# Kernel tuning notes

Measured on AMD Instinct MI355X. Metric: run time of the kernel, lower is better.

## Reference

```python
import jax, jax.numpy as jnp
import numpy as np

DIM = 512
HEADS = 8
HEAD_DIM = DIM // HEADS
SCALE = HEAD_DIM ** -0.5
B, N = 2, 4096


def setup_inputs() -> dict:
    key = jax.random.key(0)
    ks = jax.random.split(key, 7)
    s = DIM ** -0.5
    return {
        "x": jax.random.normal(ks[0], (B, N, DIM), dtype=jnp.float32),
        "qkv_w": jax.random.normal(ks[1], (DIM, 3 * DIM), dtype=jnp.float32) * s,
        "qkv_b": jax.random.normal(ks[2], (3 * DIM,), dtype=jnp.float32) * 0.01,
        "proj_w": jax.random.normal(ks[3], (DIM, DIM), dtype=jnp.float32) * s,
        "proj_b": jax.random.normal(ks[4], (DIM,), dtype=jnp.float32) * 0.01,
        "gate_w": jax.random.normal(ks[5], (DIM, HEADS), dtype=jnp.float32) * s,
        "gate_b": jax.random.normal(ks[6], (HEADS,), dtype=jnp.float32) * 0.01,
    }


def reference(x, qkv_w, qkv_b, proj_w, proj_b, gate_w, gate_b):
    b, n, c = x.shape
    qkv = x @ qkv_w + qkv_b                       # [B,N,3C]
    qkv = qkv.reshape(b, n, 3, HEADS, HEAD_DIM)
    qkv = jnp.transpose(qkv, (2, 0, 3, 1, 4))     # [3,B,H,N,hd]
    q, k, v = qkv[0], qkv[1], qkv[2]
    attn = jnp.einsum('bhnd,bhmd->bhnm', q, k) * SCALE
    attn = jax.nn.softmax(attn, axis=-1)
    y = jnp.einsum('bhnm,bhmd->bhnd', attn, v)    # [B,H,N,hd]
    gate = jax.nn.sigmoid(x @ gate_w + gate_b)    # [B,N,H] headwise
    gate = jnp.transpose(gate[..., None], (0, 2, 1, 3))  # [B,H,N,1]
    y = y * gate
    y = jnp.transpose(y, (0, 2, 1, 3)).reshape(b, n, c)
    return y @ proj_w + proj_b
```

## Files before the change

kernel.cpp:

```cpp
#include <hip/hip_runtime.h>
#include <hip/hip_bf16.h>

#define BATCH 2
#define NSEQ 4096
#define DIM 512
#define HEADS 8
#define HD 64
#define SCALE 0.125f
#define MROWS (BATCH * NSEQ)

typedef __attribute__((ext_vector_type(8))) short bf16x8;
typedef __attribute__((ext_vector_type(4))) float f32x4;

__device__ __forceinline__ short f2bf(float x) {
    unsigned u = __float_as_uint(x);
    u = (u + 0x7FFFu + ((u >> 16) & 1u)) >> 16;
    return (short)u;
}
__device__ __forceinline__ float bf2f(short s) {
    return __uint_as_float(((unsigned)(unsigned short)s) << 16);
}

__global__ __launch_bounds__(256)
void cast_kernel(const float* __restrict__ in, short* __restrict__ out) {
    const int i = (blockIdx.x * 256 + threadIdx.x) * 4;
    const float4 v = *(const float4*)(in + i);
    short4 o;
    o.x = f2bf(v.x); o.y = f2bf(v.y); o.z = f2bf(v.z); o.w = f2bf(v.w);
    *(short4*)(out + i) = o;
}

__global__ __launch_bounds__(256)
void transpose_cast_kernel(const float* __restrict__ in, short* __restrict__ out,
                           int R, int C) {
    __shared__ float tile[32][33];
    const int n0 = blockIdx.x * 32;
    const int k0 = blockIdx.y * 32;
    const int tx = threadIdx.x, ty = threadIdx.y;
    #pragma unroll
    for (int j = 0; j < 4; ++j)
        tile[ty * 4 + j][tx] = in[(size_t)(k0 + ty * 4 + j) * C + n0 + tx];
    __syncthreads();
    #pragma unroll
    for (int j = 0; j < 4; ++j)
        out[(size_t)(n0 + ty * 4 + j) * R + k0 + tx] = f2bf(tile[tx][ty * 4 + j]);
}

template<int BF16OUT>
__global__ __launch_bounds__(256)
void gemm_mfma_kernel(const short* __restrict__ A, const short* __restrict__ WT,
                      const float* __restrict__ bias,
                      float* __restrict__ C, short* __restrict__ Cb,
                      int N, int K) {
    const int m0 = blockIdx.x * 128;
    const int n0 = blockIdx.y * 128;
    const int t  = threadIdx.x;
    const int w  = t >> 6;
    const int l  = t & 63;
    const int lr = l & 15;
    const int lg = l >> 4;
    const int wm = w >> 1;
    const int wn = w & 1;

    __shared__ short As[128][72];
    __shared__ short Bs[128][72];

    f32x4 acc[4][4];
    #pragma unroll
    for (int fm = 0; fm < 4; ++fm)
        #pragma unroll
        for (int fn = 0; fn < 4; ++fn)
            acc[fm][fn] = (f32x4){0.f, 0.f, 0.f, 0.f};

    for (int k0 = 0; k0 < K; k0 += 64) {
        __syncthreads();
        #pragma unroll
        for (int i = 0; i < 4; ++i) {
            const int s   = t + i * 256;
            const int row = s >> 3, ch = s & 7;
            *(bf16x8*)&As[row][ch * 8] =
                *(const bf16x8*)(A + (size_t)(m0 + row) * K + k0 + ch * 8);
            *(bf16x8*)&Bs[row][ch * 8] =
                *(const bf16x8*)(WT + (size_t)(n0 + row) * K + k0 + ch * 8);
        }
        __syncthreads();

        #pragma unroll
        for (int kc = 0; kc < 2; ++kc) {
            bf16x8 af[4], bf[4];
            #pragma unroll
            for (int f = 0; f < 4; ++f) {
                af[f] = *(const bf16x8*)&As[wm * 64 + f * 16 + lr][kc * 32 + lg * 8];
                bf[f] = *(const bf16x8*)&Bs[wn * 64 + f * 16 + lr][kc * 32 + lg * 8];
            }
            #pragma unroll
            for (int fm = 0; fm < 4; ++fm)
                #pragma unroll
                for (int fn = 0; fn < 4; ++fn)
                    acc[fm][fn] = __builtin_amdgcn_mfma_f32_16x16x32_bf16(
                        af[fm], bf[fn], acc[fm][fn], 0, 0, 0);
        }
    }

    #pragma unroll
    for (int fm = 0; fm < 4; ++fm)
        #pragma unroll
        for (int fn = 0; fn < 4; ++fn) {
            const int col = n0 + wn * 64 + fn * 16 + lr;
            const float bb = bias[col];
            #pragma unroll
            for (int reg = 0; reg < 4; ++reg) {
                const int row = m0 + wm * 64 + fm * 16 + lg * 4 + reg;
                const float v = acc[fm][fn][reg] + bb;
                if (BF16OUT) Cb[(size_t)row * N + col] = f2bf(v);
                else         C [(size_t)row * N + col] = v;
            }
        }
}

__global__ __launch_bounds__(256)
void gate_kernel(const float* __restrict__ x, const float* __restrict__ gw,
                 const float* __restrict__ gb, float* __restrict__ gate) {
    __shared__ float gws[DIM * HEADS];
    const int t = threadIdx.x;
    #pragma unroll
    for (int i = 0; i < DIM * HEADS / (256 * 4); ++i) {
        const int s = (t + i * 256) * 4;
        *(float4*)&gws[s] = *(const float4*)(gw + s);
    }
    __syncthreads();

    const int idx = blockIdx.x * blockDim.x + t;
    const int h   = idx & 7;
    const int row = idx >> 3;
    const float* xr = x + (size_t)row * DIM;
    float acc = 0.f;
    #pragma unroll 4
    for (int k = 0; k < DIM; k += 4) {
        float4 xv = *(const float4*)(xr + k);
        acc = fmaf(xv.x, gws[(k + 0) * HEADS + h], acc);
        acc = fmaf(xv.y, gws[(k + 1) * HEADS + h], acc);
        acc = fmaf(xv.z, gws[(k + 2) * HEADS + h], acc);
        acc = fmaf(xv.w, gws[(k + 3) * HEADS + h], acc);
    }
    acc += gb[h];
    gate[idx] = 1.f / (1.f + __expf(-acc));
}

__global__ __launch_bounds__(256)
void attn_kernel(const short* __restrict__ qkvb, const float* __restrict__ gate,
                 short* __restrict__ yb) {
    const int nqt = NSEQ / 64;
    const int qt  = blockIdx.x % nqt;
    const int bh  = blockIdx.x / nqt;
    const int h   = bh % HEADS;
    const int b   = bh / HEADS;

    const int t  = threadIdx.x;
    const int w  = t >> 6;
    const int l  = t & 63;
    const int lr = l & 15;
    const int lg = l >> 4;

    __shared__ short Ks[64][72];
    __shared__ short Vt[64][72];
    __shared__ short Pw[4][16][72];

    const size_t rs = 3 * DIM;
    const short* base = qkvb + (size_t)b * NSEQ * rs;

    const short* qrow = base + (size_t)(qt * 64 + w * 16 + lr) * rs + h * HD;
    bf16x8 aq0 = *(const bf16x8*)(qrow + 0  + lg * 8);
    bf16x8 aq1 = *(const bf16x8*)(qrow + 32 + lg * 8);
    #pragma unroll
    for (int j = 0; j < 8; ++j) {
        aq0[j] = f2bf(bf2f(aq0[j]) * SCALE);
        aq1[j] = f2bf(bf2f(aq1[j]) * SCALE);
    }

    f32x4 acc_o[4];
    #pragma unroll
    for (int f = 0; f < 4; ++f) acc_o[f] = (f32x4){0.f, 0.f, 0.f, 0.f};
    float lrow[4] = {0.f, 0.f, 0.f, 0.f};

    char* pwb = (char*)&Pw[w][0][0];
    const int rswz = ((lr >> 2) & 3) << 4;
    const int rb0 = lr * 144 + ((lg * 16) ^ rswz);
    const int rb1 = lr * 144 + ((64 + lg * 16) ^ rswz);

    for (int kt = 0; kt < NSEQ / 64; ++kt) {
        __syncthreads();
        #pragma unroll
        for (int i = 0; i < 2; ++i) {
            const int s = t + i * 256;
            const int key = s >> 3, ch = s & 7;
            bf16x8 kv = *(const bf16x8*)(base + (size_t)(kt * 64 + key) * rs
                                         + DIM + h * HD + ch * 8);
            *(bf16x8*)&Ks[key][ch * 8] = kv;
        }
        {
            const int key = t & 63;
            #pragma unroll
            for (int i = 0; i < 2; ++i) {
                const int ch = (t >> 6) + 4 * i;
                bf16x8 vv = *(const bf16x8*)(base + (size_t)(kt * 64 + key) * rs
                                             + 2 * DIM + h * HD + ch * 8);
                #pragma unroll
                for (int j = 0; j < 8; ++j) Vt[ch * 8 + j][key] = vv[j];
            }
        }
        __syncthreads();

        f32x4 sfr[4];
        #pragma unroll
        for (int f = 0; f < 4; ++f) {
            f32x4 acc = (f32x4){0.f, 0.f, 0.f, 0.f};
            const bf16x8 bk0 = *(const bf16x8*)&Ks[f * 16 + lr][0  + lg * 8];
            acc = __builtin_amdgcn_mfma_f32_16x16x32_bf16(aq0, bk0, acc, 0, 0, 0);
            const bf16x8 bk1 = *(const bf16x8*)&Ks[f * 16 + lr][32 + lg * 8];
            acc = __builtin_amdgcn_mfma_f32_16x16x32_bf16(aq1, bk1, acc, 0, 0, 0);
            sfr[f] = acc;
        }

        #pragma unroll
        for (int reg = 0; reg < 4; ++reg) {
            const int row = lg * 4 + reg;
            const int wswz = ((row >> 2) & 3) << 4;
            float ls = 0.f;
            #pragma unroll
            for (int f = 0; f < 4; ++f) {
                const float pr = __expf(fminf(sfr[f][reg], 60.f));
                ls += pr;
                const int byte = row * 144 + (((f * 16 + lr) * 2) ^ wswz);
                *(short*)(pwb + byte) = f2bf(pr);
            }
            lrow[reg] += ls;
        }

        const bf16x8 ap0 = *(const bf16x8*)(pwb + rb0);
        const bf16x8 ap1 = *(const bf16x8*)(pwb + rb1);
        #pragma unroll
        for (int f2 = 0; f2 < 4; ++f2) {
            const bf16x8 bv0 = *(const bf16x8*)&Vt[f2 * 16 + lr][0  + lg * 8];
            acc_o[f2] = __builtin_amdgcn_mfma_f32_16x16x32_bf16(ap0, bv0, acc_o[f2], 0, 0, 0);
            const bf16x8 bv1 = *(const bf16x8*)&Vt[f2 * 16 + lr][32 + lg * 8];
            acc_o[f2] = __builtin_amdgcn_mfma_f32_16x16x32_bf16(ap1, bv1, acc_o[f2], 0, 0, 0);
        }
    }

    #pragma unroll
    for (int reg = 0; reg < 4; ++reg) {
        float ls = lrow[reg];
        ls += __shfl_xor(ls, 1);
        ls += __shfl_xor(ls, 2);
        ls += __shfl_xor(ls, 4);
        ls += __shfl_xor(ls, 8);
        lrow[reg] = ls;
    }
    #pragma unroll
    for (int reg = 0; reg < 4; ++reg) {
        const int row = qt * 64 + w * 16 + lg * 4 + reg;
        const float g   = gate[((size_t)b * NSEQ + row) * HEADS + h];
        const float inv = g / lrow[reg];
        #pragma unroll
        for (int f2 = 0; f2 < 4; ++f2)
            yb[((size_t)b * NSEQ + row) * DIM + h * HD + f2 * 16 + lr] =
                f2bf(acc_o[f2][reg] * inv);
    }
}

extern "C" void kernel_launch(void* const* d_in, const int* in_sizes, int n_in,
                              void* d_out, int out_size, void* d_ws, size_t ws_size,
                              hipStream_t stream) {
    const float* x      = (const float*)d_in[0];
    const float* qkv_w  = (const float*)d_in[1];
    const float* qkv_b  = (const float*)d_in[2];
    const float* proj_w = (const float*)d_in[3];
    const float* proj_b = (const float*)d_in[4];
    const float* gate_w = (const float*)d_in[5];
    const float* gate_b = (const float*)d_in[6];
    float* out = (float*)d_out;

    char* p = (char*)d_ws;
    short* x_bf    = (short*)p;  p += (size_t)MROWS * DIM * 2;
    short* qkv_wT  = (short*)p;  p += (size_t)(3 * DIM) * DIM * 2;
    short* proj_wT = (short*)p;  p += (size_t)DIM * DIM * 2;
    short* qkv_bf  = (short*)p;  p += (size_t)MROWS * (3 * DIM) * 2;
    short* yb      = (short*)p;  p += (size_t)MROWS * DIM * 2;
    float* gate    = (float*)p;

    cast_kernel<<<MROWS * DIM / 1024, 256, 0, stream>>>(x, x_bf);
    {
        dim3 blk(32, 8);
        transpose_cast_kernel<<<dim3(3 * DIM / 32, DIM / 32), blk, 0, stream>>>(
            qkv_w, qkv_wT, DIM, 3 * DIM);
        transpose_cast_kernel<<<dim3(DIM / 32, DIM / 32), blk, 0, stream>>>(
            proj_w, proj_wT, DIM, DIM);
    }
    {
        dim3 grid(MROWS / 128, 3 * DIM / 128);
        gemm_mfma_kernel<1><<<grid, 256, 0, stream>>>(x_bf, qkv_wT, qkv_b,
                                                      nullptr, qkv_bf,
                                                      3 * DIM, DIM);
    }
    gate_kernel<<<(MROWS * HEADS) / 256, 256, 0, stream>>>(x, gate_w, gate_b, gate);

    attn_kernel<<<BATCH * HEADS * (NSEQ / 64), 256, 0, stream>>>(qkv_bf, gate, yb);

    {
        dim3 grid(MROWS / 128, DIM / 128);
        gemm_mfma_kernel<0><<<grid, 256, 0, stream>>>(yb, proj_wT, proj_b,
                                                      out, nullptr,
                                                      DIM, DIM);
    }
}
```

Measured before the change: 303.1 us.

## Retile attention waves into a 2x2 grid over query rows and keys

Each of the four waves now owns 32 query rows and 32 keys for the QK^T step, then 32 rows and 32 head dims for the PV step, instead of 16 rows against the full 64 keys and dims. Per-wave shared-memory reads of K and V tiles are halved and each K/V fragment is reused across two row blocks. The cost is that the probability tile is now shared across the block through LDS with an extra barrier per key tile, and row sums are combined across waves through a small LDS buffer at the end.

```diff
diff --git a/kernel.cpp b/kernel.cpp
--- a/kernel.cpp
+++ b/kernel.cpp
@@ -161,32 +161,39 @@
     const int l  = t & 63;
     const int lr = l & 15;
     const int lg = l >> 4;
+    const int R  = w & 1;
+    const int Cq = w >> 1;
 
     __shared__ short Ks[64][72];
     __shared__ short Vt[64][72];
-    __shared__ short Pw[4][16][72];
+    __shared__ short Ps[64][72];
+    __shared__ float Lw[2][64];
 
     const size_t rs = 3 * DIM;
     const short* base = qkvb + (size_t)b * NSEQ * rs;
 
-    const short* qrow = base + (size_t)(qt * 64 + w * 16 + lr) * rs + h * HD;
-    bf16x8 aq0 = *(const bf16x8*)(qrow + 0  + lg * 8);
-    bf16x8 aq1 = *(const bf16x8*)(qrow + 32 + lg * 8);
-    #pragma unroll
-    for (int j = 0; j < 8; ++j) {
-        aq0[j] = f2bf(bf2f(aq0[j]) * SCALE);
-        aq1[j] = f2bf(bf2f(aq1[j]) * SCALE);
-    }
-
-    f32x4 acc_o[4];
-    #pragma unroll
-    for (int f = 0; f < 4; ++f) acc_o[f] = (f32x4){0.f, 0.f, 0.f, 0.f};
-    float lrow[4] = {0.f, 0.f, 0.f, 0.f};
-
-    char* pwb = (char*)&Pw[w][0][0];
-    const int rswz = ((lr >> 2) & 3) << 4;
-    const int rb0 = lr * 144 + ((lg * 16) ^ rswz);
-    const int rb1 = lr * 144 + ((64 + lg * 16) ^ rswz);
+    bf16x8 aq[2][2];
+    #pragma unroll
+    for (int rb = 0; rb < 2; ++rb) {
+        const short* qrow = base + (size_t)(qt * 64 + R * 32 + rb * 16 + lr) * rs + h * HD;
+        aq[rb][0] = *(const bf16x8*)(qrow + 0  + lg * 8);
+        aq[rb][1] = *(const bf16x8*)(qrow + 32 + lg * 8);
+        #pragma unroll
+        for (int j = 0; j < 8; ++j) {
+            aq[rb][0][j] = f2bf(bf2f(aq[rb][0][j]) * SCALE);
+            aq[rb][1][j] = f2bf(bf2f(aq[rb][1][j]) * SCALE);
+        }
+    }
+
+    f32x4 acc_o[2][2];
+    #pragma unroll
+    for (int rb = 0; rb < 2; ++rb)
+        #pragma unroll
+        for (int db = 0; db < 2; ++db)
+            acc_o[rb][db] = (f32x4){0.f, 0.f, 0.f, 0.f};
+    float lpart[2][4] = {{0.f}};
+
+    const int pswz = ((lr >> 3) & 1) << 4;
 
     for (int kt = 0; kt < NSEQ / 64; ++kt) {
         __syncthreads();
@@ -211,62 +218,102 @@
         }
         __syncthreads();
 
-        f32x4 sfr[4];
-        #pragma unroll
-        for (int f = 0; f < 4; ++f) {
-            f32x4 acc = (f32x4){0.f, 0.f, 0.f, 0.f};
-            const bf16x8 bk0 = *(const bf16x8*)&Ks[f * 16 + lr][0  + lg * 8];
-            acc = __builtin_amdgcn_mfma_f32_16x16x32_bf16(aq0, bk0, acc, 0, 0, 0);
-            const bf16x8 bk1 = *(const bf16x8*)&Ks[f * 16 + lr][32 + lg * 8];
-            acc = __builtin_amdgcn_mfma_f32_16x16x32_bf16(aq1, bk1, acc, 0, 0, 0);
-            sfr[f] = acc;
-        }
-
+        f32x4 sfr[2][2];
+        #pragma unroll
+        for (int rb = 0; rb < 2; ++rb)
+            #pragma unroll
+            for (int kb = 0; kb < 2; ++kb)
+                sfr[rb][kb] = (f32x4){0.f, 0.f, 0.f, 0.f};
+        #pragma unroll
+        for (int kc = 0; kc < 2; ++kc) {
+            bf16x8 bk[2];
+            #pragma unroll
+            for (int kb = 0; kb < 2; ++kb)
+                bk[kb] = *(const bf16x8*)&Ks[Cq * 32 + kb * 16 + lr][kc * 32 + lg * 8];
+            #pragma unroll
+            for (int rb = 0; rb < 2; ++rb)
+                #pragma unroll
+                for (int kb = 0; kb < 2; ++kb)
+                    sfr[rb][kb] = __builtin_amdgcn_mfma_f32_16x16x32_bf16(
+                        aq[rb][kc], bk[kb], sfr[rb][kb], 0, 0, 0);
+        }
+
+        #pragma unroll
+        for (int rb = 0; rb < 2; ++rb)
+            #pragma unroll
+            for (int reg = 0; reg < 4; ++reg) {
+                const int rloc = lg * 4 + reg;
+                const int row  = R * 32 + rb * 16 + rloc;
+                const int wsw  = ((rloc >> 3) & 1) << 4;
+                #pragma unroll
+                for (int kb = 0; kb < 2; ++kb) {
+                    const float pr = __expf(fminf(sfr[rb][kb][reg], 60.f));
+                    lpart[rb][reg] += pr;
+                    const int key  = Cq * 32 + kb * 16 + lr;
+                    const int byte = row * 144 + ((key * 2) ^ wsw);
+                    *(short*)((char*)Ps + byte) = f2bf(pr);
+                }
+            }
+        __syncthreads();
+
+        bf16x8 ap[2][2];
+        #pragma unroll
+        for (int rb = 0; rb < 2; ++rb)
+            #pragma unroll
+            for (int kc2 = 0; kc2 < 2; ++kc2) {
+                const int byte = (R * 32 + rb * 16 + lr) * 144
+                               + ((kc2 * 64 + lg * 16) ^ pswz);
+                ap[rb][kc2] = *(const bf16x8*)((char*)Ps + byte);
+            }
+        #pragma unroll
+        for (int kc2 = 0; kc2 < 2; ++kc2) {
+            bf16x8 bv[2];
+            #pragma unroll
+            for (int db = 0; db < 2; ++db)
+                bv[db] = *(const bf16x8*)&Vt[Cq * 32 + db * 16 + lr][kc2 * 32 + lg * 8];
+            #pragma unroll
+            for (int rb = 0; rb < 2; ++rb)
+                #pragma unroll
+                for (int db = 0; db < 2; ++db)
+                    acc_o[rb][db] = __builtin_amdgcn_mfma_f32_16x16x32_bf16(
+                        ap[rb][kc2], bv[db], acc_o[rb][db], 0, 0, 0);
+        }
+    }
+
+    #pragma unroll
+    for (int rb = 0; rb < 2; ++rb)
         #pragma unroll
         for (int reg = 0; reg < 4; ++reg) {
-            const int row = lg * 4 + reg;
-            const int wswz = ((row >> 2) & 3) << 4;
-            float ls = 0.f;
-            #pragma unroll
-            for (int f = 0; f < 4; ++f) {
-                const float pr = __expf(fminf(sfr[f][reg], 60.f));
-                ls += pr;
-                const int byte = row * 144 + (((f * 16 + lr) * 2) ^ wswz);
-                *(short*)(pwb + byte) = f2bf(pr);
-            }
-            lrow[reg] += ls;
-        }
-
-        const bf16x8 ap0 = *(const bf16x8*)(pwb + rb0);
-        const bf16x8 ap1 = *(const bf16x8*)(pwb + rb1);
-        #pragma unroll
-        for (int f2 = 0; f2 < 4; ++f2) {
-            const bf16x8 bv0 = *(const bf16x8*)&Vt[f2 * 16 + lr][0  + lg * 8];
-            acc_o[f2] = __builtin_amdgcn_mfma_f32_16x16x32_bf16(ap0, bv0, acc_o[f2], 0, 0, 0);
-            const bf16x8 bv1 = *(const bf16x8*)&Vt[f2 * 16 + lr][32 + lg * 8];
-            acc_o[f2] = __builtin_amdgcn_mfma_f32_16x16x32_bf16(ap1, bv1, acc_o[f2], 0, 0, 0);
-        }
-    }
-
-    #pragma unroll
-    for (int reg = 0; reg < 4; ++reg) {
-        float ls = lrow[reg];
-        ls += __shfl_xor(ls, 1);
-        ls += __shfl_xor(ls, 2);
-        ls += __shfl_xor(ls, 4);
-        ls += __shfl_xor(ls, 8);
-        lrow[reg] = ls;
-    }
-    #pragma unroll
-    for (int reg = 0; reg < 4; ++reg) {
-        const int row = qt * 64 + w * 16 + lg * 4 + reg;
-        const float g   = gate[((size_t)b * NSEQ + row) * HEADS + h];
-        const float inv = g / lrow[reg];
-        #pragma unroll
-        for (int f2 = 0; f2 < 4; ++f2)
-            yb[((size_t)b * NSEQ + row) * DIM + h * HD + f2 * 16 + lr] =
-                f2bf(acc_o[f2][reg] * inv);
-    }
+            float ls = lpart[rb][reg];
+            ls += __shfl_xor(ls, 1);
+            ls += __shfl_xor(ls, 2);
+            ls += __shfl_xor(ls, 4);
+            ls += __shfl_xor(ls, 8);
+            lpart[rb][reg] = ls;
+        }
+    if (lr == 0) {
+        #pragma unroll
+        for (int rb = 0; rb < 2; ++rb)
+            #pragma unroll
+            for (int reg = 0; reg < 4; ++reg)
+                Lw[Cq][R * 32 + rb * 16 + lg * 4 + reg] = lpart[rb][reg];
+    }
+    __syncthreads();
+
+    #pragma unroll
+    for (int rb = 0; rb < 2; ++rb)
+        #pragma unroll
+        for (int reg = 0; reg < 4; ++reg) {
+            const int rloc = R * 32 + rb * 16 + lg * 4 + reg;
+            const int row  = qt * 64 + rloc;
+            const float lt = Lw[0][rloc] + Lw[1][rloc];
+            const float g  = gate[((size_t)b * NSEQ + row) * HEADS + h];
+            const float inv = g / lt;
+            #pragma unroll
+            for (int db = 0; db < 2; ++db)
+                yb[((size_t)b * NSEQ + row) * DIM + h * HD + Cq * 32 + db * 16 + lr] =
+                    f2bf(acc_o[rb][db][reg] * inv);
+        }
 }
 
 extern "C" void kernel_launch(void* const* d_in, const int* in_sizes, int n_in,
```

Result: no change. 298.5 us (-1.5%).
